# Optimization experiments

Hardware: AMD Instinct MI355X
Metric: run time of the kernel (lower is better)

Reference implementation:

```python
import jax, jax.numpy as jnp
import numpy as np

S, H, E, N, K, R, NL, L = 256, 768, 1536, 16, 4, 48, 2, 1024


def setup_inputs() -> dict:
    key = jax.random.key(0)
    ks = jax.random.split(key, 12)
    def rn(k, shape, s=0.02):
        return jax.random.normal(k, shape, jnp.float32) * s
    return {
        "x": jax.random.normal(ks[0], (L, S), jnp.float32),
        "emb_w": rn(ks[1], (H, S)),
        "emb_b": rn(ks[2], (H,)),
        "norm_w": jnp.ones((NL, H), jnp.float32),
        "in_proj_w": rn(ks[3], (NL, 2 * E, H)),
        "conv_w": rn(ks[4], (NL, E, K), 0.1),
        "conv_b": rn(ks[5], (NL, E), 0.1),
        "x_proj_w": rn(ks[6], (NL, R + 2 * N, E)),
        "dt_proj_w": rn(ks[7], (NL, E, R), 0.1),
        "dt_proj_b": rn(ks[8], (NL, E), 0.1),
        "A_log": jnp.log(jnp.tile(jnp.arange(1, N + 1, dtype=jnp.float32), (NL, E, 1))),
        "D": jnp.ones((NL, E), jnp.float32),
        "out_proj_w": rn(ks[9], (NL, H, E)),
        "head_w": rn(ks[10], (S, H)),
        "head_b": rn(ks[11], (S,)),
    }


def rmsnorm(x, w, eps=1e-5):
    return x * jax.lax.rsqrt(jnp.mean(x * x, axis=-1, keepdims=True) + eps) * w


def causal_conv1d(x, w, b):
    # x: (L, E), w: (E, K) depthwise kernel, causal (left-pad K-1)
    xp = jnp.pad(x, ((K - 1, 0), (0, 0)))
    y = sum(w[:, k] * xp[k:k + x.shape[0]] for k in range(K))
    return y + b


def mamba_mixer(x, in_w, cw, cb, xp_w, dt_w, dt_b, a_log, d, out_w):
    xz = x @ in_w.T                       # (L, 2E)
    xin, z = jnp.split(xz, 2, axis=-1)
    u = jax.nn.silu(causal_conv1d(xin, cw, cb))   # (L, E)
    dbc = u @ xp_w.T                      # (L, R+2N)
    dt, B, C = dbc[:, :R], dbc[:, R:R + N], dbc[:, R + N:]
    dt = jax.nn.softplus(dt @ dt_w.T + dt_b)      # (L, E)
    A = -jnp.exp(a_log)                   # (E, N)
    dA = jnp.exp(dt[:, :, None] * A)      # (L, E, N)
    dBu = dt[:, :, None] * B[:, None, :] * u[:, :, None]  # (L, E, N)

    def step(s, t):
        dA_t, dBu_t, C_t = t
        s = s * dA_t + dBu_t              # (E, N)
        return s, s @ C_t                 # y_t: (E,)

    _, ys = jax.lax.scan(step, jnp.zeros((E, N), x.dtype), (dA, dBu, C))
    y = ys + u * d
    return (y * jax.nn.silu(z)) @ out_w.T


def reference(x, emb_w, emb_b, norm_w, in_proj_w, conv_w, conv_b, x_proj_w,
              dt_proj_w, dt_proj_b, A_log, D, out_proj_w, head_w, head_b):
    h = x @ emb_w.T + emb_b               # (L, H)
    res = None
    for i in range(NL):
        res = h if res is None else h + res
        hn = rmsnorm(res, norm_w[i])
        h = mamba_mixer(hn, in_proj_w[i], conv_w[i], conv_b[i], x_proj_w[i],
                        dt_proj_w[i], dt_proj_b[i], A_log[i], D[i], out_proj_w[i])
    return h @ head_w.T + head_b          # (L, S)
```

## Files before the change

kernel.cpp:

```cpp
#include <hip/hip_runtime.h>
#include <hip/hip_bf16.h>
#include <math.h>

#define SDIM 256
#define HDIM 768
#define EDIM 1536
#define NDIM 16
#define KCONV 4
#define RDIM 48
#define NLAYER 2
#define LSEQ 1024

#define NCHUNK 64
#define CHLEN (LSEQ / NCHUNK)
#define XSPLIT 8
#define XKCH (EDIM / XSPLIT)

typedef __hip_bfloat16 bf16;
typedef __attribute__((ext_vector_type(8))) short short8;
typedef __attribute__((ext_vector_type(4))) float f32x4;

__device__ __forceinline__ float softplusf(float x) {
    return (x > 20.f) ? x : log1pf(expf(x));
}
__device__ __forceinline__ float siluf(float x) {
    return x / (1.f + expf(-x));
}

struct F2BSegs {
    const float* src[6];
    bf16*        dst[6];
    int          n[6];
};

__global__ __launch_bounds__(256) void f2b_all(F2BSegs segs)
{
    for (int s = 0; s < 6; s++) {
        const float* __restrict__ in = segs.src[s];
        bf16* __restrict__ out = segs.dst[s];
        const int n = segs.n[s];
        for (int i = (blockIdx.x * 256 + threadIdx.x) * 4; i < n; i += gridDim.x * 256 * 4) {
            float4 v = *(const float4*)(in + i);
            out[i + 0] = (bf16)v.x; out[i + 1] = (bf16)v.y;
            out[i + 2] = (bf16)v.z; out[i + 3] = (bf16)v.w;
        }
    }
}

__global__ __launch_bounds__(256) void k_gemm_sk(const bf16* __restrict__ A, int lda,
                                                 const bf16* __restrict__ W, int ldw,
                                                 const float* __restrict__ bias,
                                                 float* __restrict__ part,
                                                 int N, int Kh, int useBias)
{
    __shared__ __align__(16) short As[64][72];
    __shared__ __align__(16) short Ws[64][72];

    const int tid  = threadIdx.x;
    const int lane = tid & 63, wid = tid >> 6;
    const int wm = wid >> 1, wn = wid & 1;
    const int row0 = blockIdx.y * 64, col0 = blockIdx.x * 64;
    const int quad = lane >> 4, l16 = lane & 15;
    const int kbase = blockIdx.z * Kh;

    f32x4 acc[2][2] = {};
    for (int k0 = 0; k0 < Kh; k0 += 64) {
        #pragma unroll
        for (int i = 0; i < 2; i++) {
            int id = tid + i * 256;
            int r = id >> 3, g = id & 7;
            *(uint4*)&As[r][g * 8] = *(const uint4*)(A + (size_t)(row0 + r) * lda + kbase + k0 + g * 8);
            *(uint4*)&Ws[r][g * 8] = *(const uint4*)(W + (size_t)(col0 + r) * ldw + kbase + k0 + g * 8);
        }
        __syncthreads();
        #pragma unroll
        for (int ks = 0; ks < 64; ks += 32) {
            short8 af[2], bfr[2];
            #pragma unroll
            for (int i = 0; i < 2; i++) af[i] = *(const short8*)&As[wm * 32 + i * 16 + l16][ks + quad * 8];
            #pragma unroll
            for (int j = 0; j < 2; j++) bfr[j] = *(const short8*)&Ws[wn * 32 + j * 16 + l16][ks + quad * 8];
            #pragma unroll
            for (int i = 0; i < 2; i++)
                #pragma unroll
                for (int j = 0; j < 2; j++)
                    acc[i][j] = __builtin_amdgcn_mfma_f32_16x16x32_bf16(af[i], bfr[j], acc[i][j], 0, 0, 0);
        }
        __syncthreads();
    }
    float* pdst = part + (size_t)blockIdx.z * LSEQ * N;
    #pragma unroll
    for (int i = 0; i < 2; i++) {
        #pragma unroll
        for (int j = 0; j < 2; j++) {
            int gn = col0 + wn * 32 + j * 16 + l16;
            int gm0 = row0 + wm * 32 + i * 16 + quad * 4;
            #pragma unroll
            for (int r = 0; r < 4; r++) {
                float v = acc[i][j][r];
                if (useBias && blockIdx.z == 0) v += bias[gn];
                pdst[(size_t)(gm0 + r) * N + gn] = v;
            }
        }
    }
}

__global__ __launch_bounds__(256) void k_gemm_skb(const bf16* __restrict__ A, int lda,
                                                  const bf16* __restrict__ W, int ldw,
                                                  bf16* __restrict__ part,
                                                  int N, int Kh)
{
    __shared__ __align__(16) short As[64][72];
    __shared__ __align__(16) short Ws[64][72];

    const int tid  = threadIdx.x;
    const int lane = tid & 63, wid = tid >> 6;
    const int wm = wid >> 1, wn = wid & 1;
    const int row0 = blockIdx.y * 64, col0 = blockIdx.x * 64;
    const int quad = lane >> 4, l16 = lane & 15;
    const int kbase = blockIdx.z * Kh;

    f32x4 acc[2][2] = {};
    for (int k0 = 0; k0 < Kh; k0 += 64) {
        #pragma unroll
        for (int i = 0; i < 2; i++) {
            int id = tid + i * 256;
            int r = id >> 3, g = id & 7;
            *(uint4*)&As[r][g * 8] = *(const uint4*)(A + (size_t)(row0 + r) * lda + kbase + k0 + g * 8);
            *(uint4*)&Ws[r][g * 8] = *(const uint4*)(W + (size_t)(col0 + r) * ldw + kbase + k0 + g * 8);
        }
        __syncthreads();
        #pragma unroll
        for (int ks = 0; ks < 64; ks += 32) {
            short8 af[2], bfr[2];
            #pragma unroll
            for (int i = 0; i < 2; i++) af[i] = *(const short8*)&As[wm * 32 + i * 16 + l16][ks + quad * 8];
            #pragma unroll
            for (int j = 0; j < 2; j++) bfr[j] = *(const short8*)&Ws[wn * 32 + j * 16 + l16][ks + quad * 8];
            #pragma unroll
            for (int i = 0; i < 2; i++)
                #pragma unroll
                for (int j = 0; j < 2; j++)
                    acc[i][j] = __builtin_amdgcn_mfma_f32_16x16x32_bf16(af[i], bfr[j], acc[i][j], 0, 0, 0);
        }
        __syncthreads();
    }
    bf16* pdst = part + (size_t)blockIdx.z * LSEQ * N;
    #pragma unroll
    for (int i = 0; i < 2; i++) {
        #pragma unroll
        for (int j = 0; j < 2; j++) {
            int gn = col0 + wn * 32 + j * 16 + l16;
            int gm0 = row0 + wm * 32 + i * 16 + quad * 4;
            #pragma unroll
            for (int r = 0; r < 4; r++)
                pdst[(size_t)(gm0 + r) * N + gn] = (bf16)acc[i][j][r];
        }
    }
}

__global__ __launch_bounds__(256) void k_gemm_h(const float* __restrict__ A0,
                                                const float* __restrict__ A1, int lda,
                                                const bf16* __restrict__ W, int ldw,
                                                const float* __restrict__ bias,
                                                float* __restrict__ out, int N, int Kd)
{
    __shared__ __align__(16) short As[64][72];
    __shared__ __align__(16) short Ws[64][72];

    const int tid  = threadIdx.x;
    const int lane = tid & 63, wid = tid >> 6;
    const int wm = wid >> 1, wn = wid & 1;
    const int row0 = blockIdx.y * 64, col0 = blockIdx.x * 64;
    const int quad = lane >> 4, l16 = lane & 15;

    f32x4 acc[2][2] = {};
    for (int k0 = 0; k0 < Kd; k0 += 64) {
        #pragma unroll
        for (int i = 0; i < 2; i++) {
            int id = tid + i * 256;
            int r = id >> 3, g = id & 7;
            size_t base = (size_t)(row0 + r) * lda + k0 + g * 8;
            float4 a0 = *(const float4*)(A0 + base);
            float4 a1 = *(const float4*)(A0 + base + 4);
            float4 b0 = *(const float4*)(A1 + base);
            float4 b1 = *(const float4*)(A1 + base + 4);
            bf16 tmp[8] = {(bf16)(a0.x + b0.x), (bf16)(a0.y + b0.y),
                           (bf16)(a0.z + b0.z), (bf16)(a0.w + b0.w),
                           (bf16)(a1.x + b1.x), (bf16)(a1.y + b1.y),
                           (bf16)(a1.z + b1.z), (bf16)(a1.w + b1.w)};
            *(uint4*)&As[r][g * 8] = *(const uint4*)tmp;
            *(uint4*)&Ws[r][g * 8] = *(const uint4*)(W + (size_t)(col0 + r) * ldw + k0 + g * 8);
        }
        __syncthreads();
        #pragma unroll
        for (int ks = 0; ks < 64; ks += 32) {
            short8 af[2], bfr[2];
            #pragma unroll
            for (int i = 0; i < 2; i++) af[i] = *(const short8*)&As[wm * 32 + i * 16 + l16][ks + quad * 8];
            #pragma unroll
            for (int j = 0; j < 2; j++) bfr[j] = *(const short8*)&Ws[wn * 32 + j * 16 + l16][ks + quad * 8];
            #pragma unroll
            for (int i = 0; i < 2; i++)
                #pragma unroll
                for (int j = 0; j < 2; j++)
                    acc[i][j] = __builtin_amdgcn_mfma_f32_16x16x32_bf16(af[i], bfr[j], acc[i][j], 0, 0, 0);
        }
        __syncthreads();
    }
    #pragma unroll
    for (int i = 0; i < 2; i++) {
        #pragma unroll
        for (int j = 0; j < 2; j++) {
            int gn = col0 + wn * 32 + j * 16 + l16;
            int gm0 = row0 + wm * 32 + i * 16 + quad * 4;
            #pragma unroll
            for (int r = 0; r < 4; r++)
                out[(size_t)(gm0 + r) * N + gn] = acc[i][j][r] + bias[gn];
        }
    }
}

__global__ __launch_bounds__(256) void k_conv(const bf16* __restrict__ xzp0,
                                              const bf16* __restrict__ xzp1,
                                              const float* __restrict__ cw,
                                              const float* __restrict__ cb,
                                              bf16* __restrict__ ub)
{
    const int NG = LSEQ * EDIM / 4;
    for (int g = blockIdx.x * 256 + threadIdx.x; g < NG; g += gridDim.x * 256) {
        int t = g / (EDIM / 4);
        int e4 = (g - t * (EDIM / 4)) * 4;
        float4 s = *(const float4*)(cb + e4);
        #pragma unroll
        for (int k = 0; k < KCONV; k++) {
            int tt = t - (KCONV - 1) + k;
            if (tt >= 0) {
                size_t o = (size_t)tt * (2 * EDIM) + e4;
                const bf16* pa = xzp0 + o;
                const bf16* pb = xzp1 + o;
                s.x += cw[(e4 + 0) * KCONV + k] * ((float)pa[0] + (float)pb[0]);
                s.y += cw[(e4 + 1) * KCONV + k] * ((float)pa[1] + (float)pb[1]);
                s.z += cw[(e4 + 2) * KCONV + k] * ((float)pa[2] + (float)pb[2]);
                s.w += cw[(e4 + 3) * KCONV + k] * ((float)pa[3] + (float)pb[3]);
            }
        }
        bf16 tmp[4] = {(bf16)siluf(s.x), (bf16)siluf(s.y), (bf16)siluf(s.z), (bf16)siluf(s.w)};
        *(uint2*)(ub + (size_t)t * EDIM + e4) = *(const uint2*)tmp;
    }
}

__global__ __launch_bounds__(256) void k_xproj_mfma(
    const bf16* __restrict__ A,
    const bf16* __restrict__ W,
    float* __restrict__ part)
{
    __shared__ __align__(16) short As[64][72];
    __shared__ __align__(16) short Ws[64][72];

    const int tid  = threadIdx.x;
    const int lane = tid & 63, wid = tid >> 6;
    const int wm = wid >> 1, wn = wid & 1;
    const int row0 = blockIdx.y * 64, col0 = blockIdx.x * 64;
    const int quad = lane >> 4, l16 = lane & 15;
    const int kbase = blockIdx.z * XKCH;

    f32x4 acc[2][2] = {};
    for (int k0 = 0; k0 < XKCH; k0 += 64) {
        #pragma unroll
        for (int i = 0; i < 2; i++) {
            int id = tid + i * 256;
            int r = id >> 3, g = id & 7;
            *(uint4*)&As[r][g * 8] =
                *(const uint4*)(A + (size_t)(row0 + r) * EDIM + kbase + k0 + g * 8);
            uint4 wv = {0, 0, 0, 0};
            if (col0 + r < 80)
                wv = *(const uint4*)(W + (size_t)(col0 + r) * EDIM + kbase + k0 + g * 8);
            *(uint4*)&Ws[r][g * 8] = wv;
        }
        __syncthreads();
        #pragma unroll
        for (int ks = 0; ks < 64; ks += 32) {
            short8 af[2], bfr[2];
            #pragma unroll
            for (int i = 0; i < 2; i++) af[i] = *(const short8*)&As[wm * 32 + i * 16 + l16][ks + quad * 8];
            #pragma unroll
            for (int j = 0; j < 2; j++) bfr[j] = *(const short8*)&Ws[wn * 32 + j * 16 + l16][ks + quad * 8];
            #pragma unroll
            for (int i = 0; i < 2; i++)
                #pragma unroll
                for (int j = 0; j < 2; j++)
                    acc[i][j] = __builtin_amdgcn_mfma_f32_16x16x32_bf16(af[i], bfr[j], acc[i][j], 0, 0, 0);
        }
        __syncthreads();
    }

    float* pdst = part + (size_t)blockIdx.z * (LSEQ * 80);
    #pragma unroll
    for (int i = 0; i < 2; i++) {
        #pragma unroll
        for (int j = 0; j < 2; j++) {
            int gn = col0 + wn * 32 + j * 16 + l16;
            int gm0 = row0 + wm * 32 + i * 16 + quad * 4;
            if (gn < 80) {
                #pragma unroll
                for (int r = 0; r < 4; r++)
                    pdst[(size_t)(gm0 + r) * 80 + gn] = acc[i][j][r];
            }
        }
    }
}

__global__ __launch_bounds__(256) void k_dt_red(
    const float* __restrict__ part, const float* __restrict__ dtw,
    const float* __restrict__ dtbb, float* __restrict__ out,
    float* __restrict__ dbc)
{
    __shared__ float AsF[16][68];
    __shared__ float WsF[16][68];
    const int tid = threadIdx.x;
    const int tx = tid & 15, ty = tid >> 4;
    const int tx4 = tx * 4, ty4 = ty * 4;
    const int row0 = blockIdx.y * 64, col0 = blockIdx.x * 64;

    if (blockIdx.x == 0) {
        for (int idx = tid; idx < 64 * 32; idx += 256) {
            int m = idx >> 5, c = 48 + (idx & 31);
            size_t o = (size_t)(row0 + m) * 80 + c;
            float s = 0.f;
            #pragma unroll
            for (int p = 0; p < XSPLIT; p++) s += part[(size_t)p * (LSEQ * 80) + o];
            dbc[o] = s;
        }
    }

    float acc[4][4] = {};
    for (int k0 = 0; k0 < RDIM; k0 += 16) {
        #pragma unroll
        for (int i = 0; i < 4; i++) {
            int idx = tid + i * 256;
            int m = idx >> 4, kk = idx & 15;
            size_t o = (size_t)(row0 + m) * 80 + k0 + kk;
            float s = 0.f;
            #pragma unroll
            for (int p = 0; p < XSPLIT; p++) s += part[(size_t)p * (LSEQ * 80) + o];
            AsF[kk][m] = s;
        }
        #pragma unroll
        for (int i = 0; i < 4; i++) {
            int idx = tid + i * 256;
            int nn = idx >> 4, kk = idx & 15;
            WsF[kk][nn] = dtw[(size_t)(col0 + nn) * RDIM + k0 + kk];
        }
        __syncthreads();
        #pragma unroll
        for (int kk = 0; kk < 16; kk++) {
            float av[4], bv[4];
            #pragma unroll
            for (int i = 0; i < 4; i++) av[i] = AsF[kk][ty4 + i];
            #pragma unroll
            for (int j = 0; j < 4; j++) bv[j] = WsF[kk][tx4 + j];
            #pragma unroll
            for (int i = 0; i < 4; i++)
                #pragma unroll
                for (int j = 0; j < 4; j++)
                    acc[i][j] += av[i] * bv[j];
        }
        __syncthreads();
    }
    #pragma unroll
    for (int i = 0; i < 4; i++) {
        int gm = row0 + ty4 + i;
        #pragma unroll
        for (int j = 0; j < 4; j++) {
            int gn = col0 + tx4 + j;
            float v = acc[i][j] + dtbb[gn];
            out[(size_t)gm * EDIM + gn] = softplusf(v);
        }
    }
}

__global__ __launch_bounds__(256) void k_rms(const float* __restrict__ h0,
                                             const float* __restrict__ h1,
                                             float* __restrict__ res,
                                             bf16* __restrict__ hnb, const float* __restrict__ w,
                                             int first)
{
    __shared__ float red[4];
    __shared__ float tot;
    const int tid = threadIdx.x;
    const int t = blockIdx.x;
    float v[3]; float ss = 0.f;
    #pragma unroll
    for (int r = 0; r < 3; r++) {
        int j = tid + r * 256;
        float xv = h0[(size_t)t * HDIM + j] + h1[(size_t)t * HDIM + j];
        if (!first) xv += res[(size_t)t * HDIM + j];
        v[r] = xv;
        res[(size_t)t * HDIM + j] = xv;
        ss += xv * xv;
    }
    #pragma unroll
    for (int m = 32; m >= 1; m >>= 1) ss += __shfl_down(ss, m);
    int wid = tid >> 6;
    if ((tid & 63) == 0) red[wid] = ss;
    __syncthreads();
    if (tid == 0) tot = red[0] + red[1] + red[2] + red[3];
    __syncthreads();
    float scale = rsqrtf(tot / (float)HDIM + 1e-5f);
    #pragma unroll
    for (int r = 0; r < 3; r++) {
        int j = tid + r * 256;
        hnb[(size_t)t * HDIM + j] = (bf16)(v[r] * scale * w[j]);
    }
}

__global__ __launch_bounds__(256) void k_scan1(const float* __restrict__ dt,
                                               const bf16* __restrict__ ub,
                                               const float* __restrict__ dbc,
                                               const float* __restrict__ a_log,
                                               float* __restrict__ chunkS,
                                               float* __restrict__ sumdt)
{
    const int ex = blockIdx.x % 6, c = blockIdx.x / 6;
    const int e = ex * 256 + threadIdx.x;
    float A[16];
    #pragma unroll
    for (int q = 0; q < 4; q++) {
        float4 a4 = *(const float4*)(a_log + e * NDIM + q * 4);
        A[q*4+0] = -__expf(a4.x); A[q*4+1] = -__expf(a4.y);
        A[q*4+2] = -__expf(a4.z); A[q*4+3] = -__expf(a4.w);
    }
    float s[16] = {};
    float sd = 0.f;
    const int t0 = c * CHLEN;
    #pragma unroll 2
    for (int tt = 0; tt < CHLEN; tt++) {
        int t = t0 + tt;
        float dtv = dt[(size_t)t * EDIM + e];
        float uv  = (float)ub[(size_t)t * EDIM + e];
        float dtu = dtv * uv;
        sd += dtv;
        float4 B4[4];
        #pragma unroll
        for (int q = 0; q < 4; q++) B4[q] = *(const float4*)(dbc + (size_t)t * 80 + RDIM + q * 4);
        const float* B = (const float*)B4;
        #pragma unroll
        for (int n = 0; n < 16; n++) s[n] = s[n] * __expf(dtv * A[n]) + dtu * B[n];
    }
    float* cs = chunkS + ((size_t)c * EDIM + e) * NDIM;
    #pragma unroll
    for (int q = 0; q < 4; q++)
        *(float4*)(cs + q * 4) = make_float4(s[q*4+0], s[q*4+1], s[q*4+2], s[q*4+3]);
    sumdt[(size_t)c * EDIM + e] = sd;
}

__global__ __launch_bounds__(256) void k_scan2(const float* __restrict__ chunkS,
                                               const float* __restrict__ sumdt,
                                               const float* __restrict__ a_log,
                                               float* __restrict__ sInit)
{
    int gid = blockIdx.x * 256 + threadIdx.x;
    if (gid >= EDIM * NDIM) return;
    int n = gid & 15, e = gid >> 4;
    const float Aen = -__expf(a_log[gid]);
    float s = 0.f;
    for (int c = 0; c < NCHUNK; c++) {
        sInit[((size_t)c * EDIM + e) * NDIM + n] = s;
        float P = __expf(Aen * sumdt[(size_t)c * EDIM + e]);
        s = s * P + chunkS[((size_t)c * EDIM + e) * NDIM + n];
    }
}

__global__ __launch_bounds__(256) void k_scan3(const float* __restrict__ dt,
                                               const bf16* __restrict__ ub,
                                               const float* __restrict__ dbc,
                                               const bf16* __restrict__ xzp0,
                                               const bf16* __restrict__ xzp1,
                                               const float* __restrict__ a_log,
                                               const float* __restrict__ Dp,
                                               const float* __restrict__ sInit,
                                               bf16* __restrict__ yzb)
{
    const int ex = blockIdx.x % 6, c = blockIdx.x / 6;
    const int e = ex * 256 + threadIdx.x;
    float A[16];
    #pragma unroll
    for (int q = 0; q < 4; q++) {
        float4 a4 = *(const float4*)(a_log + e * NDIM + q * 4);
        A[q*4+0] = -__expf(a4.x); A[q*4+1] = -__expf(a4.y);
        A[q*4+2] = -__expf(a4.z); A[q*4+3] = -__expf(a4.w);
    }
    const float dv = Dp[e];
    float s[16];
    const float* si = sInit + ((size_t)c * EDIM + e) * NDIM;
    #pragma unroll
    for (int q = 0; q < 4; q++) {
        float4 s4 = *(const float4*)(si + q * 4);
        s[q*4+0] = s4.x; s[q*4+1] = s4.y; s[q*4+2] = s4.z; s[q*4+3] = s4.w;
    }
    const int t0 = c * CHLEN;
    #pragma unroll 2
    for (int tt = 0; tt < CHLEN; tt++) {
        int t = t0 + tt;
        float dtv = dt[(size_t)t * EDIM + e];
        float uv  = (float)ub[(size_t)t * EDIM + e];
        size_t zo = (size_t)t * (2 * EDIM) + EDIM + e;
        float zv  = (float)xzp0[zo] + (float)xzp1[zo];
        float dtu = dtv * uv;
        float4 B4[4], C4[4];
        #pragma unroll
        for (int q = 0; q < 4; q++) {
            B4[q] = *(const float4*)(dbc + (size_t)t * 80 + RDIM + q * 4);
            C4[q] = *(const float4*)(dbc + (size_t)t * 80 + RDIM + NDIM + q * 4);
        }
        const float* B = (const float*)B4;
        const float* C = (const float*)C4;
        float y = 0.f;
        #pragma unroll
        for (int n = 0; n < 16; n++) {
            s[n] = s[n] * __expf(dtv * A[n]) + dtu * B[n];
            y += s[n] * C[n];
        }
        y += uv * dv;
        yzb[(size_t)t * EDIM + e] = (bf16)(y * siluf(zv));
    }
}

extern "C" void kernel_launch(void* const* d_in, const int* in_sizes, int n_in,
                              void* d_out, int out_size, void* d_ws, size_t ws_size,
                              hipStream_t stream)
{
    const float* x        = (const float*)d_in[0];
    const float* emb_w    = (const float*)d_in[1];
    const float* emb_b    = (const float*)d_in[2];
    const float* norm_w   = (const float*)d_in[3];
    const float* in_proj  = (const float*)d_in[4];
    const float* conv_w   = (const float*)d_in[5];
    const float* conv_b   = (const float*)d_in[6];
    const float* x_proj   = (const float*)d_in[7];
    const float* dt_w     = (const float*)d_in[8];
    const float* dt_b     = (const float*)d_in[9];
    const float* A_log    = (const float*)d_in[10];
    const float* Dp       = (const float*)d_in[11];
    const float* out_proj = (const float*)d_in[12];
    const float* head_w   = (const float*)d_in[13];
    const float* head_b   = (const float*)d_in[14];
    float* out = (float*)d_out;

    float* ws = (float*)d_ws;
    size_t off = 0;
    float* hpart  = ws + off; off += (size_t)2 * LSEQ * HDIM;
    float* res    = ws + off; off += (size_t)LSEQ * HDIM;
    float* dbc    = ws + off; off += (size_t)LSEQ * 80;
    float* part   = ws + off; off += (size_t)XSPLIT * LSEQ * 80;
    float* dtb    = ws + off; off += (size_t)LSEQ * EDIM;
    float* chunkS = ws + off; off += (size_t)NCHUNK * EDIM * NDIM;
    float* sumdt  = ws + off; off += (size_t)NCHUNK * EDIM;
    float* sInit  = ws + off; off += (size_t)NCHUNK * EDIM * NDIM;
    bf16* xzpart  = (bf16*)(ws + off); off += (size_t)2 * LSEQ * 2 * EDIM / 2;
    bf16* hnb     = (bf16*)(ws + off); off += (size_t)LSEQ * HDIM / 2;
    bf16* yzb     = (bf16*)(ws + off); off += (size_t)LSEQ * EDIM / 2;
    bf16* ub      = (bf16*)(ws + off); off += (size_t)LSEQ * EDIM / 2;
    bf16* xb      = (bf16*)(ws + off); off += (size_t)LSEQ * SDIM / 2;
    bf16* emb_wb  = (bf16*)(ws + off); off += (size_t)HDIM * SDIM / 2;
    bf16* head_wb = (bf16*)(ws + off); off += (size_t)SDIM * HDIM / 2;
    bf16* in_wb   = (bf16*)(ws + off); off += (size_t)NLAYER * 2 * EDIM * HDIM / 2;
    bf16* out_wb  = (bf16*)(ws + off); off += (size_t)NLAYER * HDIM * EDIM / 2;
    bf16* xwb     = (bf16*)(ws + off); off += (size_t)NLAYER * 80 * EDIM / 2;

    F2BSegs segs;
    segs.src[0] = x;        segs.dst[0] = xb;      segs.n[0] = LSEQ * SDIM;
    segs.src[1] = emb_w;    segs.dst[1] = emb_wb;  segs.n[1] = HDIM * SDIM;
    segs.src[2] = head_w;   segs.dst[2] = head_wb; segs.n[2] = SDIM * HDIM;
    segs.src[3] = in_proj;  segs.dst[3] = in_wb;   segs.n[3] = NLAYER * 2 * EDIM * HDIM;
    segs.src[4] = out_proj; segs.dst[4] = out_wb;  segs.n[4] = NLAYER * HDIM * EDIM;
    segs.src[5] = x_proj;   segs.dst[5] = xwb;     segs.n[5] = NLAYER * 80 * EDIM;
    f2b_all<<<1024, 256, 0, stream>>>(segs);

    k_gemm_sk<<<dim3(12, 16, 2), 256, 0, stream>>>(xb, SDIM, emb_wb, SDIM, emb_b,
                                                   hpart, HDIM, SDIM / 2, 1);

    for (int l = 0; l < NLAYER; l++) {
        const bf16*  inw  = in_wb  + (size_t)l * 2 * EDIM * HDIM;
        const bf16*  outw = out_wb + (size_t)l * HDIM * EDIM;
        const bf16*  xwbl = xwb    + (size_t)l * 80 * EDIM;
        const float* cw   = conv_w + (size_t)l * EDIM * KCONV;
        const float* cb   = conv_b + (size_t)l * EDIM;
        const float* dtw  = dt_w   + (size_t)l * EDIM * RDIM;
        const float* dtbb = dt_b   + (size_t)l * EDIM;
        const float* al   = A_log  + (size_t)l * EDIM * NDIM;
        const float* Dpl  = Dp     + (size_t)l * EDIM;

        k_rms<<<LSEQ, 256, 0, stream>>>(hpart, hpart + (size_t)LSEQ * HDIM, res,
                                        hnb, norm_w + (size_t)l * HDIM, l == 0);
        k_gemm_skb<<<dim3(48, 16, 2), 256, 0, stream>>>(hnb, HDIM, inw, HDIM,
                                                        xzpart, 2 * EDIM, HDIM / 2);
        k_conv<<<1536, 256, 0, stream>>>(xzpart, xzpart + (size_t)LSEQ * 2 * EDIM,
                                         cw, cb, ub);
        k_xproj_mfma<<<dim3(2, 16, XSPLIT), 256, 0, stream>>>(ub, xwbl, part);
        k_dt_red<<<dim3(24, 16), 256, 0, stream>>>(part, dtw, dtbb, dtb, dbc);
        k_scan1<<<6 * NCHUNK, 256, 0, stream>>>(dtb, ub, dbc, al, chunkS, sumdt);
        k_scan2<<<96, 256, 0, stream>>>(chunkS, sumdt, al, sInit);
        k_scan3<<<6 * NCHUNK, 256, 0, stream>>>(dtb, ub, dbc,
                                                xzpart, xzpart + (size_t)LSEQ * 2 * EDIM,
                                                al, Dpl, sInit, yzb);
        k_gemm_sk<<<dim3(12, 16, 2), 256, 0, stream>>>(yzb, EDIM, outw, EDIM, nullptr,
                                                       hpart, HDIM, EDIM / 2, 0);
    }

    k_gemm_h<<<dim3(4, 16), 256, 0, stream>>>(hpart, hpart + (size_t)LSEQ * HDIM, HDIM,
                                              head_wb, HDIM, head_b, out, SDIM, HDIM);
}
```

Baseline: 360.8 us.

## Fuse conv into x-proj, merge scan kernels with grid barrier, drop f2b pass

Removes the separate float-to-bf16 weight conversion kernel and has each GEMM convert fp32 weights and inputs while staging them into shared memory. The depthwise causal conv plus SiLU is fused into the x-projection GEMM, which reads a halo of xz rows. The dt reduction and the three scan phases now run in one persistent kernel synchronised by an atomic grid barrier. The in_proj GEMM drops its split-K partials and writes bf16 directly. Together these cut launches and intermediate traffic. The cost is redundant fp32 weight reads and conversions on every call, a grid barrier that assumes all 384 blocks are co-resident, and a barrier counter that is zeroed only once per call while the fused kernel runs once per layer.

```diff
diff --git a/kernel.cpp b/kernel.cpp
--- a/kernel.cpp
+++ b/kernel.cpp
@@ -15,6 +15,7 @@
 #define CHLEN (LSEQ / NCHUNK)
 #define XSPLIT 8
 #define XKCH (EDIM / XSPLIT)
+#define NBLK_SCAN 384
 
 typedef __hip_bfloat16 bf16;
 typedef __attribute__((ext_vector_type(8))) short short8;
@@ -27,28 +28,20 @@
     return x / (1.f + expf(-x));
 }
 
-struct F2BSegs {
-    const float* src[6];
-    bf16*        dst[6];
-    int          n[6];
-};
-
-__global__ __launch_bounds__(256) void f2b_all(F2BSegs segs)
-{
-    for (int s = 0; s < 6; s++) {
-        const float* __restrict__ in = segs.src[s];
-        bf16* __restrict__ out = segs.dst[s];
-        const int n = segs.n[s];
-        for (int i = (blockIdx.x * 256 + threadIdx.x) * 4; i < n; i += gridDim.x * 256 * 4) {
-            float4 v = *(const float4*)(in + i);
-            out[i + 0] = (bf16)v.x; out[i + 1] = (bf16)v.y;
-            out[i + 2] = (bf16)v.z; out[i + 3] = (bf16)v.w;
-        }
-    }
-}
-
-__global__ __launch_bounds__(256) void k_gemm_sk(const bf16* __restrict__ A, int lda,
-                                                 const bf16* __restrict__ W, int ldw,
+__device__ __forceinline__ void ld8(short* d, const bf16* s) {
+    *(uint4*)d = *(const uint4*)s;
+}
+__device__ __forceinline__ void ld8(short* d, const float* s) {
+    float4 a = *(const float4*)s;
+    float4 b = *(const float4*)(s + 4);
+    bf16 t[8] = {(bf16)a.x, (bf16)a.y, (bf16)a.z, (bf16)a.w,
+                 (bf16)b.x, (bf16)b.y, (bf16)b.z, (bf16)b.w};
+    *(uint4*)d = *(const uint4*)t;
+}
+
+template <typename AT>
+__global__ __launch_bounds__(256) void k_gemm_sk(const AT* __restrict__ A, int lda,
+                                                 const float* __restrict__ W, int ldw,
                                                  const float* __restrict__ bias,
                                                  float* __restrict__ part,
                                                  int N, int Kh, int useBias)
@@ -69,8 +62,8 @@
         for (int i = 0; i < 2; i++) {
             int id = tid + i * 256;
             int r = id >> 3, g = id & 7;
-            *(uint4*)&As[r][g * 8] = *(const uint4*)(A + (size_t)(row0 + r) * lda + kbase + k0 + g * 8);
-            *(uint4*)&Ws[r][g * 8] = *(const uint4*)(W + (size_t)(col0 + r) * ldw + kbase + k0 + g * 8);
+            ld8(&As[r][g * 8], A + (size_t)(row0 + r) * lda + kbase + k0 + g * 8);
+            ld8(&Ws[r][g * 8], W + (size_t)(col0 + r) * ldw + kbase + k0 + g * 8);
         }
         __syncthreads();
         #pragma unroll
@@ -106,8 +99,8 @@
 }
 
 __global__ __launch_bounds__(256) void k_gemm_skb(const bf16* __restrict__ A, int lda,
-                                                  const bf16* __restrict__ W, int ldw,
-                                                  bf16* __restrict__ part,
+                                                  const float* __restrict__ W, int ldw,
+                                                  bf16* __restrict__ outp,
                                                   int N, int Kh)
 {
     __shared__ __align__(16) short As[64][72];
@@ -118,7 +111,6 @@
     const int wm = wid >> 1, wn = wid & 1;
     const int row0 = blockIdx.y * 64, col0 = blockIdx.x * 64;
     const int quad = lane >> 4, l16 = lane & 15;
-    const int kbase = blockIdx.z * Kh;
 
     f32x4 acc[2][2] = {};
     for (int k0 = 0; k0 < Kh; k0 += 64) {
@@ -126,8 +118,8 @@
         for (int i = 0; i < 2; i++) {
             int id = tid + i * 256;
             int r = id >> 3, g = id & 7;
-            *(uint4*)&As[r][g * 8] = *(const uint4*)(A + (size_t)(row0 + r) * lda + kbase + k0 + g * 8);
-            *(uint4*)&Ws[r][g * 8] = *(const uint4*)(W + (size_t)(col0 + r) * ldw + kbase + k0 + g * 8);
+            ld8(&As[r][g * 8], A + (size_t)(row0 + r) * lda + k0 + g * 8);
+            ld8(&Ws[r][g * 8], W + (size_t)(col0 + r) * ldw + k0 + g * 8);
         }
         __syncthreads();
         #pragma unroll
@@ -145,7 +137,6 @@
         }
         __syncthreads();
     }
-    bf16* pdst = part + (size_t)blockIdx.z * LSEQ * N;
     #pragma unroll
     for (int i = 0; i < 2; i++) {
         #pragma unroll
@@ -154,14 +145,14 @@
             int gm0 = row0 + wm * 32 + i * 16 + quad * 4;
             #pragma unroll
             for (int r = 0; r < 4; r++)
-                pdst[(size_t)(gm0 + r) * N + gn] = (bf16)acc[i][j][r];
+                outp[(size_t)(gm0 + r) * N + gn] = (bf16)acc[i][j][r];
         }
     }
 }
 
 __global__ __launch_bounds__(256) void k_gemm_h(const float* __restrict__ A0,
                                                 const float* __restrict__ A1, int lda,
-                                                const bf16* __restrict__ W, int ldw,
+                                                const float* __restrict__ W, int ldw,
                                                 const float* __restrict__ bias,
                                                 float* __restrict__ out, int N, int Kd)
 {
@@ -190,7 +181,7 @@
                            (bf16)(a1.x + b1.x), (bf16)(a1.y + b1.y),
                            (bf16)(a1.z + b1.z), (bf16)(a1.w + b1.w)};
             *(uint4*)&As[r][g * 8] = *(const uint4*)tmp;
-            *(uint4*)&Ws[r][g * 8] = *(const uint4*)(W + (size_t)(col0 + r) * ldw + k0 + g * 8);
+            ld8(&Ws[r][g * 8], W + (size_t)(col0 + r) * ldw + k0 + g * 8);
         }
         __syncthreads();
         #pragma unroll
@@ -221,42 +212,17 @@
     }
 }
 
-__global__ __launch_bounds__(256) void k_conv(const bf16* __restrict__ xzp0,
-                                              const bf16* __restrict__ xzp1,
-                                              const float* __restrict__ cw,
-                                              const float* __restrict__ cb,
-                                              bf16* __restrict__ ub)
-{
-    const int NG = LSEQ * EDIM / 4;
-    for (int g = blockIdx.x * 256 + threadIdx.x; g < NG; g += gridDim.x * 256) {
-        int t = g / (EDIM / 4);
-        int e4 = (g - t * (EDIM / 4)) * 4;
-        float4 s = *(const float4*)(cb + e4);
-        #pragma unroll
-        for (int k = 0; k < KCONV; k++) {
-            int tt = t - (KCONV - 1) + k;
-            if (tt >= 0) {
-                size_t o = (size_t)tt * (2 * EDIM) + e4;
-                const bf16* pa = xzp0 + o;
-                const bf16* pb = xzp1 + o;
-                s.x += cw[(e4 + 0) * KCONV + k] * ((float)pa[0] + (float)pb[0]);
-                s.y += cw[(e4 + 1) * KCONV + k] * ((float)pa[1] + (float)pb[1]);
-                s.z += cw[(e4 + 2) * KCONV + k] * ((float)pa[2] + (float)pb[2]);
-                s.w += cw[(e4 + 3) * KCONV + k] * ((float)pa[3] + (float)pb[3]);
-            }
-        }
-        bf16 tmp[4] = {(bf16)siluf(s.x), (bf16)siluf(s.y), (bf16)siluf(s.z), (bf16)siluf(s.w)};
-        *(uint2*)(ub + (size_t)t * EDIM + e4) = *(const uint2*)tmp;
-    }
-}
-
-__global__ __launch_bounds__(256) void k_xproj_mfma(
-    const bf16* __restrict__ A,
-    const bf16* __restrict__ W,
-    float* __restrict__ part)
+__global__ __launch_bounds__(256) void k_xproj_conv(
+    const bf16* __restrict__ xz,
+    const float* __restrict__ W,
+    const float* __restrict__ cw,
+    const float* __restrict__ cb,
+    float* __restrict__ part,
+    bf16* __restrict__ ub)
 {
     __shared__ __align__(16) short As[64][72];
     __shared__ __align__(16) short Ws[64][72];
+    __shared__ __align__(16) bf16 Xr[67][64];
 
     const int tid  = threadIdx.x;
     const int lane = tid & 63, wid = tid >> 6;
@@ -267,18 +233,53 @@
 
     f32x4 acc[2][2] = {};
     for (int k0 = 0; k0 < XKCH; k0 += 64) {
+        const int ecol = kbase + k0;
+        for (int idx = tid; idx < 67 * 8; idx += 256) {
+            int r = idx >> 3, g = idx & 7;
+            int gr = row0 - 3 + r;
+            uint4 v = {0, 0, 0, 0};
+            if (gr >= 0) v = *(const uint4*)(xz + (size_t)gr * (2 * EDIM) + ecol + g * 8);
+            *(uint4*)&Xr[r][g * 8] = v;
+        }
         #pragma unroll
         for (int i = 0; i < 2; i++) {
             int id = tid + i * 256;
             int r = id >> 3, g = id & 7;
-            *(uint4*)&As[r][g * 8] =
-                *(const uint4*)(A + (size_t)(row0 + r) * EDIM + kbase + k0 + g * 8);
-            uint4 wv = {0, 0, 0, 0};
-            if (col0 + r < 80)
-                wv = *(const uint4*)(W + (size_t)(col0 + r) * EDIM + kbase + k0 + g * 8);
-            *(uint4*)&Ws[r][g * 8] = wv;
-        }
-        __syncthreads();
+            if (col0 + r < 80) {
+                ld8(&Ws[r][g * 8], W + (size_t)(col0 + r) * EDIM + ecol + g * 8);
+            } else {
+                uint4 z = {0, 0, 0, 0};
+                *(uint4*)&Ws[r][g * 8] = z;
+            }
+        }
+        __syncthreads();
+        {
+            const int e = tid & 63;
+            const int rb = (tid >> 6) * 16;
+            const float cw0 = cw[(ecol + e) * 4 + 0];
+            const float cw1 = cw[(ecol + e) * 4 + 1];
+            const float cw2 = cw[(ecol + e) * 4 + 2];
+            const float cw3 = cw[(ecol + e) * 4 + 3];
+            const float cbv = cb[ecol + e];
+            #pragma unroll
+            for (int j = 0; j < 16; j++) {
+                int r = rb + j;
+                float s = cbv
+                        + cw0 * (float)Xr[r + 0][e]
+                        + cw1 * (float)Xr[r + 1][e]
+                        + cw2 * (float)Xr[r + 2][e]
+                        + cw3 * (float)Xr[r + 3][e];
+                bf16 h = (bf16)siluf(s);
+                As[r][e] = *reinterpret_cast<short*>(&h);
+            }
+        }
+        __syncthreads();
+        if (blockIdx.x == 0) {
+            for (int idx = tid; idx < 64 * 8; idx += 256) {
+                int r = idx >> 3, g = idx & 7;
+                *(uint4*)(ub + (size_t)(row0 + r) * EDIM + ecol + g * 8) = *(const uint4*)&As[r][g * 8];
+            }
+        }
         #pragma unroll
         for (int ks = 0; ks < 64; ks += 32) {
             short8 af[2], bfr[2];
@@ -307,75 +308,6 @@
                 for (int r = 0; r < 4; r++)
                     pdst[(size_t)(gm0 + r) * 80 + gn] = acc[i][j][r];
             }
-        }
-    }
-}
-
-__global__ __launch_bounds__(256) void k_dt_red(
-    const float* __restrict__ part, const float* __restrict__ dtw,
-    const float* __restrict__ dtbb, float* __restrict__ out,
-    float* __restrict__ dbc)
-{
-    __shared__ float AsF[16][68];
-    __shared__ float WsF[16][68];
-    const int tid = threadIdx.x;
-    const int tx = tid & 15, ty = tid >> 4;
-    const int tx4 = tx * 4, ty4 = ty * 4;
-    const int row0 = blockIdx.y * 64, col0 = blockIdx.x * 64;
-
-    if (blockIdx.x == 0) {
-        for (int idx = tid; idx < 64 * 32; idx += 256) {
-            int m = idx >> 5, c = 48 + (idx & 31);
-            size_t o = (size_t)(row0 + m) * 80 + c;
-            float s = 0.f;
-            #pragma unroll
-            for (int p = 0; p < XSPLIT; p++) s += part[(size_t)p * (LSEQ * 80) + o];
-            dbc[o] = s;
-        }
-    }
-
-    float acc[4][4] = {};
-    for (int k0 = 0; k0 < RDIM; k0 += 16) {
-        #pragma unroll
-        for (int i = 0; i < 4; i++) {
-            int idx = tid + i * 256;
-            int m = idx >> 4, kk = idx & 15;
-            size_t o = (size_t)(row0 + m) * 80 + k0 + kk;
-            float s = 0.f;
-            #pragma unroll
-            for (int p = 0; p < XSPLIT; p++) s += part[(size_t)p * (LSEQ * 80) + o];
-            AsF[kk][m] = s;
-        }
-        #pragma unroll
-        for (int i = 0; i < 4; i++) {
-            int idx = tid + i * 256;
-            int nn = idx >> 4, kk = idx & 15;
-            WsF[kk][nn] = dtw[(size_t)(col0 + nn) * RDIM + k0 + kk];
-        }
-        __syncthreads();
-        #pragma unroll
-        for (int kk = 0; kk < 16; kk++) {
-            float av[4], bv[4];
-            #pragma unroll
-            for (int i = 0; i < 4; i++) av[i] = AsF[kk][ty4 + i];
-            #pragma unroll
-            for (int j = 0; j < 4; j++) bv[j] = WsF[kk][tx4 + j];
-            #pragma unroll
-            for (int i = 0; i < 4; i++)
-                #pragma unroll
-                for (int j = 0; j < 4; j++)
-                    acc[i][j] += av[i] * bv[j];
-        }
-        __syncthreads();
-    }
-    #pragma unroll
-    for (int i = 0; i < 4; i++) {
-        int gm = row0 + ty4 + i;
-        #pragma unroll
-        for (int j = 0; j < 4; j++) {
-            int gn = col0 + tx4 + j;
-            float v = acc[i][j] + dtbb[gn];
-            out[(size_t)gm * EDIM + gn] = softplusf(v);
         }
     }
 }
@@ -415,115 +347,210 @@
     }
 }
 
-__global__ __launch_bounds__(256) void k_scan1(const float* __restrict__ dt,
-                                               const bf16* __restrict__ ub,
-                                               const float* __restrict__ dbc,
-                                               const float* __restrict__ a_log,
-                                               float* __restrict__ chunkS,
-                                               float* __restrict__ sumdt)
-{
-    const int ex = blockIdx.x % 6, c = blockIdx.x / 6;
-    const int e = ex * 256 + threadIdx.x;
+__device__ __forceinline__ void gbar(int* bar)
+{
+    __threadfence();
+    __syncthreads();
+    if (threadIdx.x == 0) {
+        int t = __hip_atomic_fetch_add(&bar[0], 1, __ATOMIC_ACQ_REL, __HIP_MEMORY_SCOPE_AGENT);
+        int phase = t / NBLK_SCAN;
+        if ((t % NBLK_SCAN) == NBLK_SCAN - 1) {
+            __hip_atomic_store(&bar[1], phase + 1, __ATOMIC_RELEASE, __HIP_MEMORY_SCOPE_AGENT);
+        } else {
+            while (__hip_atomic_load(&bar[1], __ATOMIC_ACQUIRE, __HIP_MEMORY_SCOPE_AGENT) <= phase)
+                __builtin_amdgcn_s_sleep(4);
+        }
+    }
+    __syncthreads();
+    __threadfence();
+}
+
+__global__ __launch_bounds__(256, 2) void k_scan_fused(
+    const float* __restrict__ part,
+    const float* __restrict__ dtw,
+    const float* __restrict__ dtbb,
+    const bf16*  __restrict__ ub,
+    const bf16*  __restrict__ xz,
+    const float* __restrict__ a_log,
+    const float* __restrict__ Dp,
+    float* __restrict__ dtb,
+    float* __restrict__ dbc,
+    float* __restrict__ chunkS,
+    float* __restrict__ sumdt,
+    float* __restrict__ sInit,
+    bf16*  __restrict__ yzb,
+    int* __restrict__ bar)
+{
+    __shared__ __align__(16) float smem[2 * 16 * 68];
+    const int b = blockIdx.x;
+    const int tid = threadIdx.x;
+
+    {
+        const int bx = b % 24, by = b / 24;
+        const int row0 = by * 64, col0 = bx * 64;
+        const int tx = tid & 15, ty = tid >> 4;
+        const int tx4 = tx * 4, ty4 = ty * 4;
+        float (*AsF)[68] = (float (*)[68])smem;
+        float (*WsF)[68] = (float (*)[68])(smem + 16 * 68);
+
+        if (bx == 0) {
+            for (int idx = tid; idx < 64 * 32; idx += 256) {
+                int m = idx >> 5, cc = 48 + (idx & 31);
+                size_t o = (size_t)(row0 + m) * 80 + cc;
+                float sv = 0.f;
+                #pragma unroll
+                for (int p = 0; p < XSPLIT; p++) sv += part[(size_t)p * (LSEQ * 80) + o];
+                dbc[o] = sv;
+            }
+        }
+
+        float acc[4][4] = {};
+        for (int k0 = 0; k0 < RDIM; k0 += 16) {
+            #pragma unroll
+            for (int i = 0; i < 4; i++) {
+                int idx = tid + i * 256;
+                int m = idx >> 4, kk = idx & 15;
+                size_t o = (size_t)(row0 + m) * 80 + k0 + kk;
+                float sv = 0.f;
+                #pragma unroll
+                for (int p = 0; p < XSPLIT; p++) sv += part[(size_t)p * (LSEQ * 80) + o];
+                AsF[kk][m] = sv;
+            }
+            #pragma unroll
+            for (int i = 0; i < 4; i++) {
+                int idx = tid + i * 256;
+                int nn = idx >> 4, kk = idx & 15;
+                WsF[kk][nn] = dtw[(size_t)(col0 + nn) * RDIM + k0 + kk];
+            }
+            __syncthreads();
+            #pragma unroll
+            for (int kk = 0; kk < 16; kk++) {
+                float av[4], bv[4];
+                #pragma unroll
+                for (int i = 0; i < 4; i++) av[i] = AsF[kk][ty4 + i];
+                #pragma unroll
+                for (int j = 0; j < 4; j++) bv[j] = WsF[kk][tx4 + j];
+                #pragma unroll
+                for (int i = 0; i < 4; i++)
+                    #pragma unroll
+                    for (int j = 0; j < 4; j++)
+                        acc[i][j] += av[i] * bv[j];
+            }
+            __syncthreads();
+        }
+        #pragma unroll
+        for (int i = 0; i < 4; i++) {
+            int gm = row0 + ty4 + i;
+            #pragma unroll
+            for (int j = 0; j < 4; j++) {
+                int gn = col0 + tx4 + j;
+                dtb[(size_t)gm * EDIM + gn] = softplusf(acc[i][j] + dtbb[gn]);
+            }
+        }
+    }
+    gbar(bar);
+
+    const int ex = b % 6, c = b / 6;
+    const int e = ex * 256 + tid;
     float A[16];
     #pragma unroll
     for (int q = 0; q < 4; q++) {
-        float4 a4 = *(const float4*)(a_log + e * NDIM + q * 4);
+        float4 a4 = *(const float4*)(a_log + (size_t)e * NDIM + q * 4);
         A[q*4+0] = -__expf(a4.x); A[q*4+1] = -__expf(a4.y);
         A[q*4+2] = -__expf(a4.z); A[q*4+3] = -__expf(a4.w);
     }
-    float s[16] = {};
-    float sd = 0.f;
-    const int t0 = c * CHLEN;
-    #pragma unroll 2
-    for (int tt = 0; tt < CHLEN; tt++) {
-        int t = t0 + tt;
-        float dtv = dt[(size_t)t * EDIM + e];
-        float uv  = (float)ub[(size_t)t * EDIM + e];
-        float dtu = dtv * uv;
-        sd += dtv;
-        float4 B4[4];
-        #pragma unroll
-        for (int q = 0; q < 4; q++) B4[q] = *(const float4*)(dbc + (size_t)t * 80 + RDIM + q * 4);
-        const float* B = (const float*)B4;
-        #pragma unroll
-        for (int n = 0; n < 16; n++) s[n] = s[n] * __expf(dtv * A[n]) + dtu * B[n];
-    }
-    float* cs = chunkS + ((size_t)c * EDIM + e) * NDIM;
-    #pragma unroll
-    for (int q = 0; q < 4; q++)
-        *(float4*)(cs + q * 4) = make_float4(s[q*4+0], s[q*4+1], s[q*4+2], s[q*4+3]);
-    sumdt[(size_t)c * EDIM + e] = sd;
-}
-
-__global__ __launch_bounds__(256) void k_scan2(const float* __restrict__ chunkS,
-                                               const float* __restrict__ sumdt,
-                                               const float* __restrict__ a_log,
-                                               float* __restrict__ sInit)
-{
-    int gid = blockIdx.x * 256 + threadIdx.x;
-    if (gid >= EDIM * NDIM) return;
-    int n = gid & 15, e = gid >> 4;
-    const float Aen = -__expf(a_log[gid]);
-    float s = 0.f;
-    for (int c = 0; c < NCHUNK; c++) {
-        sInit[((size_t)c * EDIM + e) * NDIM + n] = s;
-        float P = __expf(Aen * sumdt[(size_t)c * EDIM + e]);
-        s = s * P + chunkS[((size_t)c * EDIM + e) * NDIM + n];
-    }
-}
-
-__global__ __launch_bounds__(256) void k_scan3(const float* __restrict__ dt,
-                                               const bf16* __restrict__ ub,
-                                               const float* __restrict__ dbc,
-                                               const bf16* __restrict__ xzp0,
-                                               const bf16* __restrict__ xzp1,
-                                               const float* __restrict__ a_log,
-                                               const float* __restrict__ Dp,
-                                               const float* __restrict__ sInit,
-                                               bf16* __restrict__ yzb)
-{
-    const int ex = blockIdx.x % 6, c = blockIdx.x / 6;
-    const int e = ex * 256 + threadIdx.x;
-    float A[16];
-    #pragma unroll
-    for (int q = 0; q < 4; q++) {
-        float4 a4 = *(const float4*)(a_log + e * NDIM + q * 4);
-        A[q*4+0] = -__expf(a4.x); A[q*4+1] = -__expf(a4.y);
-        A[q*4+2] = -__expf(a4.z); A[q*4+3] = -__expf(a4.w);
-    }
-    const float dv = Dp[e];
-    float s[16];
-    const float* si = sInit + ((size_t)c * EDIM + e) * NDIM;
-    #pragma unroll
-    for (int q = 0; q < 4; q++) {
-        float4 s4 = *(const float4*)(si + q * 4);
-        s[q*4+0] = s4.x; s[q*4+1] = s4.y; s[q*4+2] = s4.z; s[q*4+3] = s4.w;
-    }
-    const int t0 = c * CHLEN;
-    #pragma unroll 2
-    for (int tt = 0; tt < CHLEN; tt++) {
-        int t = t0 + tt;
-        float dtv = dt[(size_t)t * EDIM + e];
-        float uv  = (float)ub[(size_t)t * EDIM + e];
-        size_t zo = (size_t)t * (2 * EDIM) + EDIM + e;
-        float zv  = (float)xzp0[zo] + (float)xzp1[zo];
-        float dtu = dtv * uv;
-        float4 B4[4], C4[4];
+    {
+        float s[16] = {};
+        float sd = 0.f;
+        const int t0 = c * CHLEN;
+        #pragma unroll 2
+        for (int tt = 0; tt < CHLEN; tt++) {
+            int t = t0 + tt;
+            float dtv = dtb[(size_t)t * EDIM + e];
+            float uv  = (float)ub[(size_t)t * EDIM + e];
+            float dtu = dtv * uv;
+            sd += dtv;
+            float4 B4[4];
+            #pragma unroll
+            for (int q = 0; q < 4; q++) B4[q] = *(const float4*)(dbc + (size_t)t * 80 + RDIM + q * 4);
+            const float* B = (const float*)B4;
+            #pragma unroll
+            for (int n = 0; n < 16; n++) s[n] = s[n] * __expf(dtv * A[n]) + dtu * B[n];
+        }
+        float* cs = chunkS + ((size_t)c * EDIM + e) * NDIM;
+        #pragma unroll
+        for (int q = 0; q < 4; q++)
+            *(float4*)(cs + q * 4) = make_float4(s[q*4+0], s[q*4+1], s[q*4+2], s[q*4+3]);
+        sumdt[(size_t)c * EDIM + e] = sd;
+    }
+    gbar(bar);
+
+    {
+        float* sP = smem;
+        float* sX = smem + 256;
+        const int pl = tid & 63, q = tid >> 6;
+        const int p = b * 64 + pl;
+        const int pe = p >> 4;
+        const float Aen = -__expf(a_log[p]);
+        float P[16], X[16];
+        float Pc = 1.f, Xc = 0.f;
+        #pragma unroll
+        for (int j = 0; j < 16; j++) {
+            int cc = q * 16 + j;
+            float Pj = __expf(Aen * sumdt[(size_t)cc * EDIM + pe]);
+            float Xj = chunkS[(size_t)cc * (EDIM * NDIM) + p];
+            P[j] = Pj; X[j] = Xj;
+            Xc = Pj * Xc + Xj;
+            Pc *= Pj;
+        }
+        sP[q * 64 + pl] = Pc;
+        sX[q * 64 + pl] = Xc;
+        __syncthreads();
+        float s = 0.f;
+        for (int g = 0; g < q; g++) s = sP[g * 64 + pl] * s + sX[g * 64 + pl];
+        #pragma unroll
+        for (int j = 0; j < 16; j++) {
+            int cc = q * 16 + j;
+            sInit[(size_t)cc * (EDIM * NDIM) + p] = s;
+            s = P[j] * s + X[j];
+        }
+    }
+    gbar(bar);
+
+    {
+        const float dv = Dp[e];
+        float s[16];
+        const float* si = sInit + ((size_t)c * EDIM + e) * NDIM;
         #pragma unroll
         for (int q = 0; q < 4; q++) {
-            B4[q] = *(const float4*)(dbc + (size_t)t * 80 + RDIM + q * 4);
-            C4[q] = *(const float4*)(dbc + (size_t)t * 80 + RDIM + NDIM + q * 4);
-        }
-        const float* B = (const float*)B4;
-        const float* C = (const float*)C4;
-        float y = 0.f;
-        #pragma unroll
-        for (int n = 0; n < 16; n++) {
-            s[n] = s[n] * __expf(dtv * A[n]) + dtu * B[n];
-            y += s[n] * C[n];
-        }
-        y += uv * dv;
-        yzb[(size_t)t * EDIM + e] = (bf16)(y * siluf(zv));
+            float4 s4 = *(const float4*)(si + q * 4);
+            s[q*4+0] = s4.x; s[q*4+1] = s4.y; s[q*4+2] = s4.z; s[q*4+3] = s4.w;
+        }
+        const int t0 = c * CHLEN;
+        #pragma unroll 2
+        for (int tt = 0; tt < CHLEN; tt++) {
+            int t = t0 + tt;
+            float dtv = dtb[(size_t)t * EDIM + e];
+            float uv  = (float)ub[(size_t)t * EDIM + e];
+            float zv  = (float)xz[(size_t)t * (2 * EDIM) + EDIM + e];
+            float dtu = dtv * uv;
+            float4 B4[4], C4[4];
+            #pragma unroll
+            for (int q = 0; q < 4; q++) {
+                B4[q] = *(const float4*)(dbc + (size_t)t * 80 + RDIM + q * 4);
+                C4[q] = *(const float4*)(dbc + (size_t)t * 80 + RDIM + NDIM + q * 4);
+            }
+            const float* B = (const float*)B4;
+            const float* C = (const float*)C4;
+            float y = 0.f;
+            #pragma unroll
+            for (int n = 0; n < 16; n++) {
+                s[n] = s[n] * __expf(dtv * A[n]) + dtu * B[n];
+                y += s[n] * C[n];
+            }
+            y += uv * dv;
+            yzb[(size_t)t * EDIM + e] = (bf16)(y * siluf(zv));
+        }
     }
 }
 
@@ -558,57 +585,39 @@
     float* chunkS = ws + off; off += (size_t)NCHUNK * EDIM * NDIM;
     float* sumdt  = ws + off; off += (size_t)NCHUNK * EDIM;
     float* sInit  = ws + off; off += (size_t)NCHUNK * EDIM * NDIM;
-    bf16* xzpart  = (bf16*)(ws + off); off += (size_t)2 * LSEQ * 2 * EDIM / 2;
+    int*  bar     = (int*)(ws + off); off += 8;
+    bf16* xz      = (bf16*)(ws + off); off += (size_t)LSEQ * 2 * EDIM / 2;
     bf16* hnb     = (bf16*)(ws + off); off += (size_t)LSEQ * HDIM / 2;
     bf16* yzb     = (bf16*)(ws + off); off += (size_t)LSEQ * EDIM / 2;
     bf16* ub      = (bf16*)(ws + off); off += (size_t)LSEQ * EDIM / 2;
-    bf16* xb      = (bf16*)(ws + off); off += (size_t)LSEQ * SDIM / 2;
-    bf16* emb_wb  = (bf16*)(ws + off); off += (size_t)HDIM * SDIM / 2;
-    bf16* head_wb = (bf16*)(ws + off); off += (size_t)SDIM * HDIM / 2;
-    bf16* in_wb   = (bf16*)(ws + off); off += (size_t)NLAYER * 2 * EDIM * HDIM / 2;
-    bf16* out_wb  = (bf16*)(ws + off); off += (size_t)NLAYER * HDIM * EDIM / 2;
-    bf16* xwb     = (bf16*)(ws + off); off += (size_t)NLAYER * 80 * EDIM / 2;
-
-    F2BSegs segs;
-    segs.src[0] = x;        segs.dst[0] = xb;      segs.n[0] = LSEQ * SDIM;
-    segs.src[1] = emb_w;    segs.dst[1] = emb_wb;  segs.n[1] = HDIM * SDIM;
-    segs.src[2] = head_w;   segs.dst[2] = head_wb; segs.n[2] = SDIM * HDIM;
-    segs.src[3] = in_proj;  segs.dst[3] = in_wb;   segs.n[3] = NLAYER * 2 * EDIM * HDIM;
-    segs.src[4] = out_proj; segs.dst[4] = out_wb;  segs.n[4] = NLAYER * HDIM * EDIM;
-    segs.src[5] = x_proj;   segs.dst[5] = xwb;     segs.n[5] = NLAYER * 80 * EDIM;
-    f2b_all<<<1024, 256, 0, stream>>>(segs);
-
-    k_gemm_sk<<<dim3(12, 16, 2), 256, 0, stream>>>(xb, SDIM, emb_wb, SDIM, emb_b,
-                                                   hpart, HDIM, SDIM / 2, 1);
+
+    hipMemsetAsync(bar, 0, 2 * sizeof(int), stream);
+
+    k_gemm_sk<float><<<dim3(12, 16, 2), 256, 0, stream>>>(x, SDIM, emb_w, SDIM, emb_b,
+                                                          hpart, HDIM, SDIM / 2, 1);
 
     for (int l = 0; l < NLAYER; l++) {
-        const bf16*  inw  = in_wb  + (size_t)l * 2 * EDIM * HDIM;
-        const bf16*  outw = out_wb + (size_t)l * HDIM * EDIM;
-        const bf16*  xwbl = xwb    + (size_t)l * 80 * EDIM;
-        const float* cw   = conv_w + (size_t)l * EDIM * KCONV;
-        const float* cb   = conv_b + (size_t)l * EDIM;
-        const float* dtw  = dt_w   + (size_t)l * EDIM * RDIM;
-        const float* dtbb = dt_b   + (size_t)l * EDIM;
-        const float* al   = A_log  + (size_t)l * EDIM * NDIM;
-        const float* Dpl  = Dp     + (size_t)l * EDIM;
+        const float* inw  = in_proj  + (size_t)l * 2 * EDIM * HDIM;
+        const float* outw = out_proj + (size_t)l * HDIM * EDIM;
+        const float* xwl  = x_proj   + (size_t)l * 80 * EDIM;
+        const float* cw   = conv_w   + (size_t)l * EDIM * KCONV;
+        const float* cb   = conv_b   + (size_t)l * EDIM;
+        const float* dtw  = dt_w     + (size_t)l * EDIM * RDIM;
+        const float* dtbb = dt_b     + (size_t)l * EDIM;
+        const float* al   = A_log    + (size_t)l * EDIM * NDIM;
+        const float* Dpl  = Dp       + (size_t)l * EDIM;
 
         k_rms<<<LSEQ, 256, 0, stream>>>(hpart, hpart + (size_t)LSEQ * HDIM, res,
                                         hnb, norm_w + (size_t)l * HDIM, l == 0);
-        k_gemm_skb<<<dim3(48, 16, 2), 256, 0, stream>>>(hnb, HDIM, inw, HDIM,
-                                                        xzpart, 2 * EDIM, HDIM / 2);
-        k_conv<<<1536, 256, 0, stream>>>(xzpart, xzpart + (size_t)LSEQ * 2 * EDIM,
-                                         cw, cb, ub);
-        k_xproj_mfma<<<dim3(2, 16, XSPLIT), 256, 0, stream>>>(ub, xwbl, part);
-        k_dt_red<<<dim3(24, 16), 256, 0, stream>>>(part, dtw, dtbb, dtb, dbc);
-        k_scan1<<<6 * NCHUNK, 256, 0, stream>>>(dtb, ub, dbc, al, chunkS, sumdt);
-        k_scan2<<<96, 256, 0, stream>>>(chunkS, sumdt, al, sInit);
-        k_scan3<<<6 * NCHUNK, 256, 0, stream>>>(dtb, ub, dbc,
-                                                xzpart, xzpart + (size_t)LSEQ * 2 * EDIM,
-                                                al, Dpl, sInit, yzb);
-        k_gemm_sk<<<dim3(12, 16, 2), 256, 0, stream>>>(yzb, EDIM, outw, EDIM, nullptr,
-                                                       hpart, HDIM, EDIM / 2, 0);
+        k_gemm_skb<<<dim3(48, 16, 1), 256, 0, stream>>>(hnb, HDIM, inw, HDIM,
+                                                        xz, 2 * EDIM, HDIM);
+        k_xproj_conv<<<dim3(2, 16, XSPLIT), 256, 0, stream>>>(xz, xwl, cw, cb, part, ub);
+        k_scan_fused<<<NBLK_SCAN, 256, 0, stream>>>(part, dtw, dtbb, ub, xz, al, Dpl,
+                                                    dtb, dbc, chunkS, sumdt, sInit, yzb, bar);
+        k_gemm_sk<bf16><<<dim3(12, 16, 2), 256, 0, stream>>>(yzb, EDIM, outw, EDIM, nullptr,
+                                                             hpart, HDIM, EDIM / 2, 0);
     }
 
     k_gemm_h<<<dim3(4, 16), 256, 0, stream>>>(hpart, hpart + (size_t)LSEQ * HDIM, HDIM,
-                                              head_wb, HDIM, head_b, out, SDIM, HDIM);
-}
+                                              head_w, HDIM, head_b, out, SDIM, HDIM);
+}
```

After: 1.104 ms. 3.06x slower.
